# Optimization experiments

Measured on AMD Instinct MI355X. Metric: run time of the kernel, lower is better.

The kernel has to match this reference:

```python
import jax, jax.numpy as jnp
import numpy as np

NEG_INF = -1e30  # stands in for float('-inf') masked_fill; safe under softmax
MAX_ITERS = 6


def setup_inputs() -> dict:
    key = jax.random.key(0)
    ks = jax.random.split(key, 8)
    B, T, D, Dp, E = 8, 1500, 1536, 1024, 192
    s = lambda fan_in: 1.0 / np.sqrt(fan_in)
    return {
        "h": jax.random.normal(ks[0], (B, T, D), jnp.float32),
        "W1": jax.random.normal(ks[1], (3 * D, Dp), jnp.float32) * s(3 * D),
        "Wc": jax.random.normal(ks[2], (D, Dp), jnp.float32) * s(D),
        "W2": jax.random.normal(ks[3], (Dp, D), jnp.float32) * s(Dp),
        "b2": jnp.zeros((D,), jnp.float32),
        "w0": jax.random.normal(ks[4], (2 * D, E), jnp.float32) * s(2 * D),
        "b0": jnp.zeros((E,), jnp.float32),
        "Wstop": jax.random.normal(ks[5], (2 * D, 1), jnp.float32) * s(2 * D),
        "bstop": jnp.zeros((1,), jnp.float32),
        "threshold": jnp.full((1,), 0.5, jnp.float32),
        "C0": jnp.zeros((D,), jnp.float32),
    }


def _weighted_stats(h, a):
    # h: [B,T,D], a broadcastable to [B,T,D]
    mu = jnp.sum(a * h, axis=1)                         # [B,D]
    second = jnp.sum(a * h * h, axis=1)                 # [B,D]
    sigma = jnp.sqrt(jnp.clip(second - mu * mu, 1e-8))
    return mu, sigma


def reference(h, W1, Wc, W2, b2, w0, b0, Wstop, bstop, threshold, C0):
    B, T, D = h.shape
    th = threshold[0]

    # a_init = 1/T is constant across iterations -> hoist uniform stats and W1(e)
    mu0, sigma0 = _weighted_stats(h, jnp.float32(1.0 / T))          # [B,D]
    e = jnp.concatenate(
        [h,
         jnp.broadcast_to(mu0[:, None, :], (B, T, D)),
         jnp.broadcast_to(sigma0[:, None, :], (B, T, D))], axis=-1)  # [B,T,3D]
    base = jnp.einsum('btk,kp->btp', e, W1)                          # [B,T,Dp]

    energy_mask = jnp.mean(h * h, axis=-1) > 1e-4                    # [B,T]

    C = jnp.broadcast_to(C0[None, :], (B, D))
    stop = jnp.zeros((B,), bool)
    mask = jnp.ones((B, MAX_ITERS), bool)
    iters = jnp.arange(MAX_ITERS)

    embs, probs = [], []
    for i in range(MAX_ITERS):
        out1 = base + (C @ Wc)[:, None, :]                           # [B,T,Dp]
        out2 = jax.nn.relu(out1) @ W2 + b2                           # [B,T,D]
        att_raw = jnp.mean(out2, axis=-1)                            # [B,T]
        att_raw = jnp.where(energy_mask, att_raw, NEG_INF)
        A = jax.nn.softmax(att_raw, axis=-1)
        A = A / (jnp.sum(A, axis=1, keepdims=True) + 1e-8)

        # NOTE: faithful to source -- second weighted_stats uses out2 ('a'), not A
        mu_p, sigma_p = _weighted_stats(h, out2)                     # [B,D]
        emb = jnp.concatenate([mu_p, sigma_p], axis=-1) @ w0 + b0    # [B,E]
        emb = emb / jnp.maximum(
            jnp.linalg.norm(emb, axis=-1, keepdims=True), 1e-12)

        active = (~stop).astype(h.dtype)[:, None]
        C = C + active * (jnp.einsum('bt,btd->bd', A, h) / T)

        z = jnp.concatenate([jnp.sum(A[:, :, None] * out2, axis=1), C], axis=-1)
        p = jax.nn.sigmoid(z @ Wstop + bstop)[:, 0]                  # [B]

        newly = p < th
        mask = mask & ~(newly[:, None] & (iters[None, :] >= i))
        stop = stop | newly
        embs.append(emb)
        probs.append(p)

    E = jnp.stack(embs, axis=1)                                      # [B,6,E]
    E = E * mask[:, :, None].astype(E.dtype)
    P = jnp.stack(probs, axis=1)                                     # [B,6]
    return E, P
```

## Files before the change

### kernel.cpp

```cpp
#include <hip/hip_runtime.h>
#include <math.h>

#define NB 8
#define NT 1500
#define ND 1536
#define NP 1024
#define NE 192
#define NITER 6
#define NEGINF -1e30f

typedef __attribute__((ext_vector_type(8))) short bf16x8;
typedef __attribute__((ext_vector_type(4))) float f32x4;
typedef __attribute__((ext_vector_type(8))) unsigned short us16x8;

__device__ __forceinline__ unsigned short bf_rne(float x) {
    unsigned u = __float_as_uint(x);
    return (unsigned short)((u + 0x7FFFu + ((u >> 16) & 1u)) >> 16);
}
__device__ __forceinline__ float bf_f(unsigned short u) {
    return __uint_as_float(((unsigned)u) << 16);
}

__device__ __forceinline__ float block_reduce_sum(float v, float* red) {
    int tid = threadIdx.x;
    red[tid] = v; __syncthreads();
    for (int s = blockDim.x >> 1; s > 0; s >>= 1) {
        if (tid < s) red[tid] += red[tid + s];
        __syncthreads();
    }
    float r = red[0]; __syncthreads();
    return r;
}

__global__ void k_colstats(const float* __restrict__ h, float* __restrict__ sum1,
                           float* __restrict__ sum2) {
    int d = blockIdx.x * 256 + threadIdx.x;
    int b = blockIdx.y;
    int t0 = blockIdx.z * 125, t1 = t0 + 125;
    const float* hp = h + (size_t)b * NT * ND + d;
    float s = 0.f, s2 = 0.f;
    for (int t = t0; t < t1; ++t) { float v = hp[(size_t)t * ND]; s += v; s2 += v * v; }
    atomicAdd(&sum1[b * ND + d], s);
    atomicAdd(&sum2[b * ND + d], s2);
}

__global__ void k_stats_fin(float* __restrict__ mu0, float* __restrict__ sig0) {
    int i = blockIdx.x * 256 + threadIdx.x;
    float mu = mu0[i] * (1.f / NT);
    float sec = sig0[i] * (1.f / NT);
    mu0[i] = mu;
    sig0[i] = sqrtf(fmaxf(sec - mu * mu, 1e-8f));
}

__global__ void k_w2r(const float* __restrict__ W2, const float* __restrict__ b2,
                      float* __restrict__ w2r, float* __restrict__ b2m) {
    __shared__ float red[256];
    int p = blockIdx.x;
    float s = 0.f;
    if (p < NP) {
        const float* row = W2 + (size_t)p * ND;
        for (int d = threadIdx.x; d < ND; d += 256) s += row[d];
        s = block_reduce_sum(s, red);
        if (threadIdx.x == 0) w2r[p] = s * (1.f / ND);
    } else {
        for (int d = threadIdx.x; d < ND; d += 256) s += b2[d];
        s = block_reduce_sum(s, red);
        if (threadIdx.x == 0) b2m[0] = s * (1.f / ND);
    }
}

__global__ void k_biasb(const float* __restrict__ W1, const float* __restrict__ mu0,
                        const float* __restrict__ sig0, float* __restrict__ biasb) {
    int p = blockIdx.x * 256 + threadIdx.x;
    int d0 = blockIdx.y * 16, d1 = d0 + 16;
    float acc[NB];
#pragma unroll
    for (int b = 0; b < NB; ++b) acc[b] = 0.f;
    for (int d = d0; d < d1; ++d) {
        float wa = W1[(size_t)(ND + d) * NP + p];
        float wb = W1[(size_t)(2 * ND + d) * NP + p];
#pragma unroll
        for (int b = 0; b < NB; ++b)
            acc[b] += mu0[b * ND + d] * wa + sig0[b * ND + d] * wb;
    }
#pragma unroll
    for (int b = 0; b < NB; ++b) atomicAdd(&biasb[b * NP + p], acc[b]);
}

__global__ void k_init(float* __restrict__ C, const float* __restrict__ C0,
                       float* __restrict__ stopf) {
    int d = blockIdx.x * 256 + threadIdx.x;
    int b = blockIdx.y;
    C[b * ND + d] = C0[d];
    if (blockIdx.x == 0 && threadIdx.x == 0) stopf[b] = 0.f;
}

__global__ void k_split_w(const float* __restrict__ W, int ldw, int kcnt,
                          unsigned short* __restrict__ th, unsigned short* __restrict__ tl) {
    __shared__ float t[128][33];
    int nt = blockIdx.x, kc = blockIdx.y, tid = threadIdx.x;
    int col = tid & 127, kh = tid >> 7;
    const float* wp = W + (size_t)(kc * 32 + kh) * ldw + nt * 128 + col;
#pragma unroll
    for (int i = 0; i < 16; ++i)
        t[col][kh + 2 * i] = wp[(size_t)(2 * i) * ldw];
    __syncthreads();
    int r = tid >> 1;
    int swz = (r >> 1) & 3;
    size_t tb = ((size_t)nt * kcnt + kc) * 4096;
#pragma unroll
    for (int j = 0; j < 2; ++j) {
        int so = (tid & 1) * 2 + j;
        int s = so ^ swz;
        us16x8 hv, lv;
#pragma unroll
        for (int q = 0; q < 8; ++q) {
            float x = t[r][s * 8 + q];
            unsigned short hh = bf_rne(x);
            hv[q] = hh;
            lv[q] = bf_rne(x - bf_f(hh));
        }
        *(us16x8*)&th[tb + r * 32 + so * 8] = hv;
        *(us16x8*)&tl[tb + r * 32 + so * 8] = lv;
    }
}

__global__ void k_split_h(const float* __restrict__ h, unsigned short* __restrict__ th,
                          float* __restrict__ energy) {
    int tr = blockIdx.x, kc = blockIdx.y, b = blockIdx.z;
    int tid = threadIdx.x;
    int r = tid >> 1, quad = tid & 1;
    int row = tr * 128 + r;
    bool ok = row < NT;
    size_t tb = ((size_t)(b * 12 + tr) * 48 + kc) * 4096;
    const float* hp = h + ((size_t)b * NT + (ok ? row : 0)) * ND + kc * 32 + quad * 16;
    int swz = (r >> 1) & 3;
    float es = 0.f;
#pragma unroll
    for (int half = 0; half < 2; ++half) {
        us16x8 hv;
#pragma unroll
        for (int j = 0; j < 2; ++j) {
            float x0 = 0.f, x1 = 0.f, x2 = 0.f, x3 = 0.f;
            if (ok) {
                float4 v = *(const float4*)(hp + half * 8 + j * 4);
                x0 = v.x; x1 = v.y; x2 = v.z; x3 = v.w;
                es += x0 * x0 + x1 * x1 + x2 * x2 + x3 * x3;
            }
            hv[j * 4 + 0] = bf_rne(x0); hv[j * 4 + 1] = bf_rne(x1);
            hv[j * 4 + 2] = bf_rne(x2); hv[j * 4 + 3] = bf_rne(x3);
        }
        int off = r * 32 + (((quad * 2 + half) ^ swz) << 3);
        *(us16x8*)&th[tb + off] = hv;
    }
    es += __shfl_xor(es, 1);
    if (ok && quad == 0) atomicAdd(&energy[b * NT + row], es);
}

__global__ void k_relu_att(const unsigned short* __restrict__ base16,
                           const float* __restrict__ cvec, const float* __restrict__ w2r,
                           unsigned short* __restrict__ th, float* __restrict__ att) {
    int tr = blockIdx.x, kc = blockIdx.y, b = blockIdx.z;
    int tid = threadIdx.x;
    int r = tid >> 1, quad = tid & 1;
    int row = tr * 128 + r;
    bool ok = row < NT;
    size_t tb = ((size_t)(b * 12 + tr) * 32 + kc) * 4096;
    const unsigned short* bp = base16 + ((size_t)b * NT + (ok ? row : 0)) * NP + kc * 32 + quad * 16;
    const float* cv = cvec + b * NP + kc * 32 + quad * 16;
    const float* wr = w2r + kc * 32 + quad * 16;
    int swz = (r >> 1) & 3;
    float asum = 0.f;
#pragma unroll
    for (int half = 0; half < 2; ++half) {
        us16x8 bv = (us16x8){0, 0, 0, 0, 0, 0, 0, 0};
        if (ok) bv = *(const us16x8*)(bp + half * 8);
        us16x8 hv;
#pragma unroll
        for (int j = 0; j < 2; ++j) {
            float4 c4 = *(const float4*)(cv + half * 8 + j * 4);
            float4 w4 = *(const float4*)(wr + half * 8 + j * 4);
            float x0 = fmaxf(bf_f(bv[j * 4 + 0]) + c4.x, 0.f);
            float x1 = fmaxf(bf_f(bv[j * 4 + 1]) + c4.y, 0.f);
            float x2 = fmaxf(bf_f(bv[j * 4 + 2]) + c4.z, 0.f);
            float x3 = fmaxf(bf_f(bv[j * 4 + 3]) + c4.w, 0.f);
            if (ok) asum += x0 * w4.x + x1 * w4.y + x2 * w4.z + x3 * w4.w;
            hv[j * 4 + 0] = bf_rne(x0); hv[j * 4 + 1] = bf_rne(x1);
            hv[j * 4 + 2] = bf_rne(x2); hv[j * 4 + 3] = bf_rne(x3);
        }
        int off = r * 32 + (((quad * 2 + half) ^ swz) << 3);
        *(us16x8*)&th[tb + off] = hv;
    }
    asum += __shfl_xor(asum, 1);
    if (ok && quad == 0) atomicAdd(&att[b * NT + row], asum);
}

__global__ __launch_bounds__(256, 4) void k_gemm_relu(
    const unsigned short* __restrict__ ht, const unsigned short* __restrict__ at_h,
    const unsigned short* __restrict__ bt_h, const float* __restrict__ b2,
    const float* __restrict__ Aw, float* __restrict__ part) {
    constexpr int KC = NP / 32;
    __shared__ __align__(16) unsigned short As[2][4096];
    __shared__ __align__(16) unsigned short Bs[2][4096];
    int flat = blockIdx.x + 12 * (blockIdx.y + 12 * blockIdx.z);
    int swzf = (flat & 7) * 144 + (flat >> 3);
    int tr = swzf % 12, nt = (swzf / 12) % 12, b = swzf / 144;
    int tid = threadIdx.x;
    int lane = tid & 63, w = tid >> 6;
    int wr = w >> 1, wc = w & 1;
    int l15 = lane & 15, kg = lane >> 4;
    int sw = (l15 >> 1) & 3;
    f32x4 acc[4][4];
#pragma unroll
    for (int m = 0; m < 4; ++m)
#pragma unroll
        for (int n = 0; n < 4; ++n) acc[m][n] = (f32x4){0.f, 0.f, 0.f, 0.f};
    int aoff[4], boff[4];
#pragma unroll
    for (int m = 0; m < 4; ++m) aoff[m] = (wr * 64 + m * 16 + l15) * 32 + ((kg ^ sw) << 3);
#pragma unroll
    for (int n = 0; n < 4; ++n) boff[n] = (wc * 64 + n * 16 + l15) * 32 + ((kg ^ sw) << 3);

    const unsigned short* ga = at_h + ((size_t)(b * 12 + tr) * KC) * 4096 + lane * 8;
    const unsigned short* gb = bt_h + ((size_t)nt * KC) * 4096 + lane * 8;

    auto stage = [&](int buf, int kc) {
#pragma unroll
        for (int c = 0; c < 4; ++c) {
            int seg = w * 4 + c;
            int part_ = seg & 7;
            const unsigned short* src = ((seg >> 3) == 0 ? ga : gb) + (size_t)kc * 4096 + part_ * 512;
            unsigned short* dst = ((seg >> 3) == 0 ? &As[buf][0] : &Bs[buf][0]) + part_ * 512;
            __builtin_amdgcn_global_load_lds(src, dst, 16, 0, 0);
        }
    };

    stage(0, 0);
    __syncthreads();
    int cur = 0;
    for (int kc = 0; kc < KC; ++kc) {
        if (kc + 1 < KC) stage(cur ^ 1, kc + 1);
        bf16x8 af[4], bfr[4];
#pragma unroll
        for (int m = 0; m < 4; ++m) af[m] = *(const bf16x8*)&As[cur][aoff[m]];
#pragma unroll
        for (int n = 0; n < 4; ++n) bfr[n] = *(const bf16x8*)&Bs[cur][boff[n]];
#pragma unroll
        for (int n = 0; n < 4; ++n)
#pragma unroll
            for (int m = 0; m < 4; ++m)
                acc[m][n] = __builtin_amdgcn_mfma_f32_16x16x32_bf16(af[m], bfr[n], acc[m][n], 0, 0, 0);
        __syncthreads();
        cur ^= 1;
    }

    int rowb = tr * 128 + wr * 64 + (kg << 2);
    int colb = nt * 128 + wc * 64 + l15;
    const unsigned short* htb = ht + (size_t)(b * 12 + tr) * 48 * 4096;
    float b2c[4];
#pragma unroll
    for (int n = 0; n < 4; ++n) b2c[n] = b2[colb + n * 16];
    float pm[4] = {0, 0, 0, 0}, ps2[4] = {0, 0, 0, 0}, pza[4] = {0, 0, 0, 0}, pah[4] = {0, 0, 0, 0};
#pragma unroll
    for (int m = 0; m < 4; ++m) {
#pragma unroll
        for (int q = 0; q < 4; ++q) {
            int row = rowb + m * 16 + q;
            int r_in = wr * 64 + (kg << 2) + m * 16 + q;
            bool ok = row < NT;
            float okf = ok ? 1.f : 0.f;
            float a = Aw[b * NT + (ok ? row : (NT - 1))] * okf;
            int rsw = (r_in >> 1) & 3;
#pragma unroll
            for (int n = 0; n < 4; ++n) {
                int col = colb + n * 16;
                float hv = bf_f(htb[(size_t)(col >> 5) * 4096 + r_in * 32 +
                                    ((((col & 31) >> 3) ^ rsw) << 3) + (col & 7)]) * okf;
                float o2 = acc[m][n][q] + b2c[n];
                pm[n] = fmaf(o2, hv, pm[n]);
                ps2[n] = fmaf(o2 * hv, hv, ps2[n]);
                pza[n] = fmaf(a, o2, pza[n]);
                pah[n] = fmaf(a, hv, pah[n]);
            }
        }
    }
#pragma unroll
    for (int n = 0; n < 4; ++n) {
        pm[n] += __shfl_xor(pm[n], 16); pm[n] += __shfl_xor(pm[n], 32);
        ps2[n] += __shfl_xor(ps2[n], 16); ps2[n] += __shfl_xor(ps2[n], 32);
        pza[n] += __shfl_xor(pza[n], 16); pza[n] += __shfl_xor(pza[n], 32);
        pah[n] += __shfl_xor(pah[n], 16); pah[n] += __shfl_xor(pah[n], 32);
        if (kg == 0) {
            int col = colb + n * 16;
            size_t pb = (((size_t)(tr * 2 + wr) * NB + b) * 4) * ND;
            part[pb + 0 * (size_t)ND + col] = pm[n];
            part[pb + 1 * (size_t)ND + col] = ps2[n];
            part[pb + 2 * (size_t)ND + col] = pza[n];
            part[pb + 3 * (size_t)ND + col] = pah[n];
        }
    }
}

__global__ void k_redsum(const float* __restrict__ part, float* __restrict__ red4) {
    int idx = blockIdx.x * 256 + threadIdx.x;
    int b = idx / ND, d = idx % ND;
    float s0 = 0.f, s1 = 0.f, s2 = 0.f, s3 = 0.f;
    for (int s = 0; s < 24; ++s) {
        const float* p = part + (((size_t)s * NB + b) * 4) * ND + d;
        s0 += p[0];
        s1 += p[(size_t)ND];
        s2 += p[2 * (size_t)ND];
        s3 += p[3 * (size_t)ND];
    }
    red4[idx] = s0;
    red4[(size_t)NB * ND + idx] = s1;
    red4[3 * (size_t)NB * ND + idx] = s2;
    red4[2 * (size_t)NB * ND + idx] = s3;
}

__global__ __launch_bounds__(256, 3) void k_gemm_base(
    const unsigned short* __restrict__ ht, const unsigned short* __restrict__ bt_h,
    const unsigned short* __restrict__ bt_l, const float* __restrict__ biasb,
    unsigned short* __restrict__ Out16) {
    constexpr int KC2 = ND / 64;
    __shared__ __align__(16) unsigned short As[8192];
    __shared__ __align__(16) unsigned short Bh_s[8192];
    __shared__ __align__(16) unsigned short Bl_s[8192];
    int flat = blockIdx.x + 12 * (blockIdx.y + 8 * blockIdx.z);
    int swzf = (flat & 7) * 96 + (flat >> 3);
    int tr = swzf % 12, nt = (swzf / 12) % 8, b = swzf / 96;
    int tid = threadIdx.x;
    int lane = tid & 63, w = tid >> 6;
    int wr = w >> 1, wc = w & 1;
    int l15 = lane & 15, kg = lane >> 4;
    int sw = (l15 >> 1) & 3;
    f32x4 acc[4][4];
#pragma unroll
    for (int m = 0; m < 4; ++m)
#pragma unroll
        for (int n = 0; n < 4; ++n) acc[m][n] = (f32x4){0.f, 0.f, 0.f, 0.f};
    int aoff[4], boff[4];
#pragma unroll
    for (int m = 0; m < 4; ++m) aoff[m] = (wr * 64 + m * 16 + l15) * 32 + ((kg ^ sw) << 3);
#pragma unroll
    for (int n = 0; n < 4; ++n) boff[n] = (wc * 64 + n * 16 + l15) * 32 + ((kg ^ sw) << 3);

    const unsigned short* ga = ht + ((size_t)(b * 12 + tr) * 48) * 4096 + lane * 8;
    const unsigned short* gbh = bt_h + ((size_t)nt * 48) * 4096 + lane * 8;
    const unsigned short* gbl = bt_l + ((size_t)nt * 48) * 4096 + lane * 8;

    for (int kc2 = 0; kc2 < KC2; ++kc2) {
#pragma unroll
        for (int c = 0; c < 12; ++c) {
            int seg = w * 12 + c;
            int part = seg & 15, mat = seg >> 4;
            const unsigned short* src =
                (mat == 0 ? ga : mat == 1 ? gbh : gbl) + (size_t)kc2 * 8192 + part * 512;
            unsigned short* dst =
                (mat == 0 ? &As[0] : mat == 1 ? &Bh_s[0] : &Bl_s[0]) + part * 512;
            __builtin_amdgcn_global_load_lds(src, dst, 16, 0, 0);
        }
        __syncthreads();
#pragma unroll
        for (int half = 0; half < 2; ++half) {
            int ho = half * 4096;
            bf16x8 af[4];
#pragma unroll
            for (int m = 0; m < 4; ++m) af[m] = *(const bf16x8*)&As[ho + aoff[m]];
#pragma unroll
            for (int n = 0; n < 4; ++n) {
                bf16x8 bh = *(const bf16x8*)&Bh_s[ho + boff[n]];
                bf16x8 bl = *(const bf16x8*)&Bl_s[ho + boff[n]];
#pragma unroll
                for (int m = 0; m < 4; ++m) {
                    acc[m][n] = __builtin_amdgcn_mfma_f32_16x16x32_bf16(af[m], bh, acc[m][n], 0, 0, 0);
                    acc[m][n] = __builtin_amdgcn_mfma_f32_16x16x32_bf16(af[m], bl, acc[m][n], 0, 0, 0);
                }
            }
        }
        __syncthreads();
    }

    int rowb = tr * 128 + wr * 64 + (kg << 2);
    int colb = nt * 128 + wc * 64 + l15;
#pragma unroll
    for (int m = 0; m < 4; ++m)
#pragma unroll
        for (int q = 0; q < 4; ++q) {
            int row = rowb + m * 16 + q;
            if (row < NT) {
                unsigned short* orow = Out16 + ((size_t)b * NT + row) * NP;
#pragma unroll
                for (int n = 0; n < 4; ++n)
                    orow[colb + n * 16] =
                        bf_rne(acc[m][n][q] + biasb[b * NP + colb + n * 16]);
            }
        }
}

__global__ void k_cvec(const float* __restrict__ C, const float* __restrict__ Wc,
                       float* __restrict__ cvec) {
    int p = blockIdx.x * 256 + threadIdx.x;
    int d0 = blockIdx.y * 48, d1 = d0 + 48;
    float acc[NB];
#pragma unroll
    for (int b = 0; b < NB; ++b) acc[b] = 0.f;
    for (int d = d0; d < d1; ++d) {
        float wc = Wc[(size_t)d * NP + p];
#pragma unroll
        for (int b = 0; b < NB; ++b) acc[b] += C[b * ND + d] * wc;
    }
#pragma unroll
    for (int b = 0; b < NB; ++b) atomicAdd(&cvec[b * NP + p], acc[b]);
}

__global__ void k_softmax(const float* __restrict__ att, const float* __restrict__ energy,
                          const float* __restrict__ b2m, float* __restrict__ A) {
    __shared__ float red[256];
    int b = blockIdx.x, tid = threadIdx.x;
    float bm = b2m[0];
    const float* x = att + (size_t)b * NT;
    const float* en = energy + (size_t)b * NT;
    float* a = A + (size_t)b * NT;
    float mx = -3.4e38f;
    for (int t = tid; t < NT; t += 256) {
        float v = (en[t] * (1.f / ND) > 1e-4f) ? x[t] + bm : NEGINF;
        mx = fmaxf(mx, v);
    }
    red[tid] = mx; __syncthreads();
    for (int s = 128; s > 0; s >>= 1) {
        if (tid < s) red[tid] = fmaxf(red[tid], red[tid + s]);
        __syncthreads();
    }
    mx = red[0]; __syncthreads();
    float sm = 0.f;
    for (int t = tid; t < NT; t += 256) {
        float v = (en[t] * (1.f / ND) > 1e-4f) ? x[t] + bm : NEGINF;
        float e = expf(v - mx); a[t] = e; sm += e;
    }
    float s1 = block_reduce_sum(sm, red);
    float inv1 = 1.f / s1;
    float sm2 = 0.f;
    for (int t = tid; t < NT; t += 256) { float v = a[t] * inv1; a[t] = v; sm2 += v; }
    float s2 = block_reduce_sum(sm2, red);
    float inv2 = 1.f / (s2 + 1e-8f);
    for (int t = tid; t < NT; t += 256) a[t] *= inv2;
}

__global__ void k_embacc(const float* __restrict__ red4, const float* __restrict__ w0,
                         float* __restrict__ embt) {
    __shared__ float mus[NB][48], sgs[NB][48];
    int e = threadIdx.x;
    int d0 = blockIdx.x * 48;
    const float* mup = red4;
    const float* s2p = red4 + (size_t)NB * ND;
    for (int idx = e; idx < NB * 48; idx += 192) {
        int b = idx / 48, dd = idx % 48;
        float mu = mup[b * ND + d0 + dd];
        mus[b][dd] = mu;
        sgs[b][dd] = sqrtf(fmaxf(s2p[b * ND + d0 + dd] - mu * mu, 1e-8f));
    }
    __syncthreads();
    float acc[NB];
#pragma unroll
    for (int b = 0; b < NB; ++b) acc[b] = 0.f;
    for (int dd = 0; dd < 48; ++dd) {
        float wa = w0[(size_t)(d0 + dd) * NE + e];
        float wb = w0[(size_t)(ND + d0 + dd) * NE + e];
#pragma unroll
        for (int b = 0; b < NB; ++b)
            acc[b] += mus[b][dd] * wa + sgs[b][dd] * wb;
    }
#pragma unroll
    for (int b = 0; b < NB; ++b) atomicAdd(&embt[b * NE + e], acc[b]);
}

__global__ void k_tail2(const float* __restrict__ red4, const float* __restrict__ embt,
                        const float* __restrict__ b0, const float* __restrict__ Wstop,
                        const float* __restrict__ bstop, const float* __restrict__ thr,
                        float* __restrict__ Cb, float* __restrict__ stopf,
                        float* __restrict__ Eout, float* __restrict__ Pout, int iter) {
    __shared__ float red[256];
    __shared__ float liveflag;
    int b = blockIdx.x, tid = threadIdx.x;
    const float* Ahb = red4 + (size_t)2 * NB * ND + b * ND;
    const float* zAb = red4 + (size_t)3 * NB * ND + b * ND;
    float active = (stopf[b] > 0.5f) ? 0.f : 1.f;
    float dsum = 0.f;
    for (int d = tid; d < ND; d += 256) {
        float Cn = Cb[b * ND + d] + active * (Ahb[d] * (1.f / NT));
        Cb[b * ND + d] = Cn;
        dsum += zAb[d] * Wstop[d] + Cn * Wstop[ND + d];
    }
    float s = block_reduce_sum(dsum, red);
    if (tid == 0) {
        float logit = s + bstop[0];
        float p = 1.f / (1.f + expf(-logit));
        Pout[b * NITER + iter] = p;
        bool newly = p < thr[0];
        if (newly) stopf[b] = 1.f;
        liveflag = (active > 0.5f && !newly) ? 1.f : 0.f;
    }
    __syncthreads();
    float live = liveflag;
    float emb = (tid < NE) ? (embt[b * NE + tid] + b0[tid]) : 0.f;
    float nrm = block_reduce_sum(emb * emb, red);
    float sc = live / fmaxf(sqrtf(nrm), 1e-12f);
    if (tid < NE) Eout[((size_t)b * NITER + iter) * NE + tid] = emb * sc;
}

extern "C" void kernel_launch(void* const* d_in, const int* in_sizes, int n_in,
                              void* d_out, int out_size, void* d_ws, size_t ws_size,
                              hipStream_t stream) {
    const float* h = (const float*)d_in[0];
    const float* W1 = (const float*)d_in[1];
    const float* Wc = (const float*)d_in[2];
    const float* W2 = (const float*)d_in[3];
    const float* b2 = (const float*)d_in[4];
    const float* w0 = (const float*)d_in[5];
    const float* b0 = (const float*)d_in[6];
    const float* Wstop = (const float*)d_in[7];
    const float* bstop = (const float*)d_in[8];
    const float* thr = (const float*)d_in[9];
    const float* C0 = (const float*)d_in[10];

    float* Eout = (float*)d_out;
    float* Pout = Eout + (size_t)NB * NITER * NE;

    char* wsb = (char*)d_ws;
    size_t off = 0;
    auto alloc = [&](size_t bytes) -> void* {
        void* p = wsb + off; off += (bytes + 15) & ~(size_t)15; return p;
    };

    unsigned short* base16 = (unsigned short*)alloc((size_t)NB * NT * NP * 2);
    unsigned short* rel_h = (unsigned short*)alloc((size_t)NB * 12 * 32 * 4096 * 2);
    unsigned short* ht_h = (unsigned short*)alloc((size_t)NB * 12 * 48 * 4096 * 2);
    unsigned short* w1t_h = (unsigned short*)alloc((size_t)8 * 48 * 4096 * 2);
    unsigned short* w1t_l = (unsigned short*)alloc((size_t)8 * 48 * 4096 * 2);
    unsigned short* w2t_h = (unsigned short*)alloc((size_t)12 * 32 * 4096 * 2);
    unsigned short* w2t_l = (unsigned short*)alloc((size_t)12 * 32 * 4096 * 2);
    size_t pz = (size_t)2 * NB * ND + NB * NT + NB * NP;
    float* mu0 = (float*)alloc(pz * 4);
    float* sig0 = mu0 + NB * ND;
    float* energy = sig0 + NB * ND;
    float* biasb = energy + NB * NT;
    float* w2r = (float*)alloc(NP * 4);
    float* b2m = (float*)alloc(16);
    size_t zelems = (size_t)NB * NP + NB * NT + NB * NE;
    float* cvec = (float*)alloc(zelems * 4);
    float* att = cvec + NB * NP;
    float* embt = att + NB * NT;
    float* red4 = (float*)alloc((size_t)4 * NB * ND * 4);
    float* part = (float*)alloc((size_t)24 * NB * 4 * ND * 4);
    float* Abuf = (float*)alloc(NB * NT * 4);
    float* Cb = (float*)alloc(NB * ND * 4);
    float* stopf = (float*)alloc(32);
    size_t zero_bytes = zelems * 4;

    hipMemsetAsync(mu0, 0, pz * 4, stream);
    k_colstats<<<dim3(ND / 256, NB, 12), 256, 0, stream>>>(h, mu0, sig0);
    k_stats_fin<<<dim3(NB * ND / 256), 256, 0, stream>>>(mu0, sig0);
    k_w2r<<<dim3(NP + 1), 256, 0, stream>>>(W2, b2, w2r, b2m);
    k_biasb<<<dim3(4, 96), 256, 0, stream>>>(W1, mu0, sig0, biasb);
    k_split_w<<<dim3(8, 48), 256, 0, stream>>>(W1, NP, 48, w1t_h, w1t_l);
    k_split_w<<<dim3(12, 32), 256, 0, stream>>>(W2, ND, 32, w2t_h, w2t_l);
    k_split_h<<<dim3(12, 48, NB), 256, 0, stream>>>(h, ht_h, energy);
    k_gemm_base<<<dim3(12, 8, NB), 256, 0, stream>>>(ht_h, w1t_h, w1t_l, biasb, base16);
    k_init<<<dim3(ND / 256, NB), 256, 0, stream>>>(Cb, C0, stopf);

    for (int i = 0; i < NITER; ++i) {
        hipMemsetAsync(cvec, 0, zero_bytes, stream);
        k_cvec<<<dim3(4, 32), 256, 0, stream>>>(Cb, Wc, cvec);
        k_relu_att<<<dim3(12, 32, NB), 256, 0, stream>>>(base16, cvec, w2r, rel_h, att);
        k_softmax<<<dim3(NB), 256, 0, stream>>>(att, energy, b2m, Abuf);
        k_gemm_relu<<<dim3(12, 12, NB), 256, 0, stream>>>(
            ht_h, rel_h, w2t_h, b2, Abuf, part);
        k_redsum<<<dim3(48), 256, 0, stream>>>(part, red4);
        k_embacc<<<dim3(32), 192, 0, stream>>>(red4, w0, embt);
        k_tail2<<<dim3(NB), 256, 0, stream>>>(red4, embt, b0, Wstop, bstop, thr,
                                              Cb, stopf, Eout, Pout, i);
    }
}
```

Measured before the change: 1.107 ms.

## Fuse relu(base+cvec) into GEMM A-tile staging, drop relu tile buffer

```diff
diff --git a/kernel.cpp b/kernel.cpp
--- a/kernel.cpp
+++ b/kernel.cpp
@@ -157,51 +157,41 @@
     if (ok && quad == 0) atomicAdd(&energy[b * NT + row], es);
 }
 
-__global__ void k_relu_att(const unsigned short* __restrict__ base16,
-                           const float* __restrict__ cvec, const float* __restrict__ w2r,
-                           unsigned short* __restrict__ th, float* __restrict__ att) {
-    int tr = blockIdx.x, kc = blockIdx.y, b = blockIdx.z;
-    int tid = threadIdx.x;
-    int r = tid >> 1, quad = tid & 1;
-    int row = tr * 128 + r;
-    bool ok = row < NT;
-    size_t tb = ((size_t)(b * 12 + tr) * 32 + kc) * 4096;
-    const unsigned short* bp = base16 + ((size_t)b * NT + (ok ? row : 0)) * NP + kc * 32 + quad * 16;
-    const float* cv = cvec + b * NP + kc * 32 + quad * 16;
-    const float* wr = w2r + kc * 32 + quad * 16;
-    int swz = (r >> 1) & 3;
-    float asum = 0.f;
-#pragma unroll
-    for (int half = 0; half < 2; ++half) {
-        us16x8 bv = (us16x8){0, 0, 0, 0, 0, 0, 0, 0};
-        if (ok) bv = *(const us16x8*)(bp + half * 8);
-        us16x8 hv;
-#pragma unroll
-        for (int j = 0; j < 2; ++j) {
-            float4 c4 = *(const float4*)(cv + half * 8 + j * 4);
-            float4 w4 = *(const float4*)(wr + half * 8 + j * 4);
-            float x0 = fmaxf(bf_f(bv[j * 4 + 0]) + c4.x, 0.f);
-            float x1 = fmaxf(bf_f(bv[j * 4 + 1]) + c4.y, 0.f);
-            float x2 = fmaxf(bf_f(bv[j * 4 + 2]) + c4.z, 0.f);
-            float x3 = fmaxf(bf_f(bv[j * 4 + 3]) + c4.w, 0.f);
-            if (ok) asum += x0 * w4.x + x1 * w4.y + x2 * w4.z + x3 * w4.w;
-            hv[j * 4 + 0] = bf_rne(x0); hv[j * 4 + 1] = bf_rne(x1);
-            hv[j * 4 + 2] = bf_rne(x2); hv[j * 4 + 3] = bf_rne(x3);
-        }
-        int off = r * 32 + (((quad * 2 + half) ^ swz) << 3);
-        *(us16x8*)&th[tb + off] = hv;
-    }
-    asum += __shfl_xor(asum, 1);
-    if (ok && quad == 0) atomicAdd(&att[b * NT + row], asum);
+__global__ void k_att(const unsigned short* __restrict__ base16,
+                      const float* __restrict__ cvec, const float* __restrict__ w2r,
+                      float* __restrict__ att) {
+    __shared__ float cv_sh[NP], wr_sh[NP];
+    int blk = blockIdx.x, b = blockIdx.y;
+    int tid = threadIdx.x, lane = tid & 63, wv = tid >> 6;
+    for (int i = tid; i < NP / 4; i += 256) {
+        ((float4*)cv_sh)[i] = ((const float4*)(cvec + (size_t)b * NP))[i];
+        ((float4*)wr_sh)[i] = ((const float4*)w2r)[i];
+    }
+    __syncthreads();
+    int row = blk * 4 + wv;
+    const unsigned short* bp = base16 + ((size_t)b * NT + row) * NP + lane * 16;
+    us16x8 v0 = *(const us16x8*)bp;
+    us16x8 v1 = *(const us16x8*)(bp + 8);
+    float s = 0.f;
+#pragma unroll
+    for (int j = 0; j < 8; ++j)
+        s += fmaxf(bf_f(v0[j]) + cv_sh[lane * 16 + j], 0.f) * wr_sh[lane * 16 + j];
+#pragma unroll
+    for (int j = 0; j < 8; ++j)
+        s += fmaxf(bf_f(v1[j]) + cv_sh[lane * 16 + 8 + j], 0.f) * wr_sh[lane * 16 + 8 + j];
+#pragma unroll
+    for (int d = 1; d < 64; d <<= 1) s += __shfl_xor(s, d);
+    if (lane == 0) att[b * NT + row] = s;
 }
 
 __global__ __launch_bounds__(256, 4) void k_gemm_relu(
-    const unsigned short* __restrict__ ht, const unsigned short* __restrict__ at_h,
-    const unsigned short* __restrict__ bt_h, const float* __restrict__ b2,
-    const float* __restrict__ Aw, float* __restrict__ part) {
+    const unsigned short* __restrict__ base16, const float* __restrict__ cvec,
+    const unsigned short* __restrict__ ht, const unsigned short* __restrict__ bt_h,
+    const float* __restrict__ b2, const float* __restrict__ Aw, float* __restrict__ part) {
     constexpr int KC = NP / 32;
     __shared__ __align__(16) unsigned short As[2][4096];
     __shared__ __align__(16) unsigned short Bs[2][4096];
+    __shared__ float cv_sh[NP];
     int flat = blockIdx.x + 12 * (blockIdx.y + 12 * blockIdx.z);
     int swzf = (flat & 7) * 144 + (flat >> 3);
     int tr = swzf % 12, nt = (swzf / 12) % 12, b = swzf / 144;
@@ -221,25 +211,61 @@
 #pragma unroll
     for (int n = 0; n < 4; ++n) boff[n] = (wc * 64 + n * 16 + l15) * 32 + ((kg ^ sw) << 3);
 
-    const unsigned short* ga = at_h + ((size_t)(b * 12 + tr) * KC) * 4096 + lane * 8;
     const unsigned short* gb = bt_h + ((size_t)nt * KC) * 4096 + lane * 8;
 
-    auto stage = [&](int buf, int kc) {
-#pragma unroll
-        for (int c = 0; c < 4; ++c) {
-            int seg = w * 4 + c;
-            int part_ = seg & 7;
-            const unsigned short* src = ((seg >> 3) == 0 ? ga : gb) + (size_t)kc * 4096 + part_ * 512;
-            unsigned short* dst = ((seg >> 3) == 0 ? &As[buf][0] : &Bs[buf][0]) + part_ * 512;
+    int r2 = tid >> 1, quad = tid & 1;
+    int arow = tr * 128 + r2;
+    int rowc = arow < NT ? arow : (NT - 1);
+    int aswz = (r2 >> 1) & 3;
+    const unsigned short* ap = base16 + ((size_t)b * NT + rowc) * NP + quad * 16;
+
+    for (int i = tid; i < NP / 4; i += 256)
+        ((float4*)cv_sh)[i] = ((const float4*)(cvec + (size_t)b * NP))[i];
+    __syncthreads();
+
+    auto stageB = [&](int buf, int kc) {
+#pragma unroll
+        for (int c = 0; c < 2; ++c) {
+            int seg = w * 2 + c;
+            const unsigned short* src = gb + (size_t)kc * 4096 + seg * 512;
+            unsigned short* dst = &Bs[buf][0] + seg * 512;
             __builtin_amdgcn_global_load_lds(src, dst, 16, 0, 0);
         }
     };
-
-    stage(0, 0);
+    auto loadA = [&](int kc, us16x8* raw) {
+        raw[0] = *(const us16x8*)(ap + kc * 32);
+        raw[1] = *(const us16x8*)(ap + kc * 32 + 8);
+    };
+    auto writeA = [&](int buf, const us16x8* raw, int kc) {
+#pragma unroll
+        for (int half = 0; half < 2; ++half) {
+            us16x8 hv;
+#pragma unroll
+            for (int j = 0; j < 8; ++j) {
+                float x = bf_f(raw[half][j]) + cv_sh[kc * 32 + quad * 16 + half * 8 + j];
+                hv[j] = bf_rne(fmaxf(x, 0.f));
+            }
+            int so = quad * 2 + half;
+            int off = r2 * 32 + ((so ^ aswz) << 3);
+            *(us16x8*)&As[buf][off] = hv;
+        }
+    };
+
+    {
+        us16x8 raw0[2];
+        stageB(0, 0);
+        loadA(0, raw0);
+        writeA(0, raw0, 0);
+    }
     __syncthreads();
     int cur = 0;
     for (int kc = 0; kc < KC; ++kc) {
-        if (kc + 1 < KC) stage(cur ^ 1, kc + 1);
+        bool np = kc + 1 < KC;
+        us16x8 rawn[2];
+        if (np) {
+            stageB(cur ^ 1, kc + 1);
+            loadA(kc + 1, rawn);
+        }
         bf16x8 af[4], bfr[4];
 #pragma unroll
         for (int m = 0; m < 4; ++m) af[m] = *(const bf16x8*)&As[cur][aoff[m]];
@@ -250,6 +276,7 @@
 #pragma unroll
             for (int m = 0; m < 4; ++m)
                 acc[m][n] = __builtin_amdgcn_mfma_f32_16x16x32_bf16(af[m], bfr[n], acc[m][n], 0, 0, 0);
+        if (np) writeA(cur ^ 1, rawn, kc + 1);
         __syncthreads();
         cur ^= 1;
     }
@@ -534,7 +561,6 @@
     };
 
     unsigned short* base16 = (unsigned short*)alloc((size_t)NB * NT * NP * 2);
-    unsigned short* rel_h = (unsigned short*)alloc((size_t)NB * 12 * 32 * 4096 * 2);
     unsigned short* ht_h = (unsigned short*)alloc((size_t)NB * 12 * 48 * 4096 * 2);
     unsigned short* w1t_h = (unsigned short*)alloc((size_t)8 * 48 * 4096 * 2);
     unsigned short* w1t_l = (unsigned short*)alloc((size_t)8 * 48 * 4096 * 2);
@@ -547,10 +573,10 @@
     float* biasb = energy + NB * NT;
     float* w2r = (float*)alloc(NP * 4);
     float* b2m = (float*)alloc(16);
-    size_t zelems = (size_t)NB * NP + NB * NT + NB * NE;
+    size_t zelems = (size_t)NB * NP + NB * NE;
     float* cvec = (float*)alloc(zelems * 4);
-    float* att = cvec + NB * NP;
-    float* embt = att + NB * NT;
+    float* embt = cvec + NB * NP;
+    float* att = (float*)alloc((size_t)NB * NT * 4);
     float* red4 = (float*)alloc((size_t)4 * NB * ND * 4);
     float* part = (float*)alloc((size_t)24 * NB * 4 * ND * 4);
     float* Abuf = (float*)alloc(NB * NT * 4);
@@ -572,10 +598,10 @@
     for (int i = 0; i < NITER; ++i) {
         hipMemsetAsync(cvec, 0, zero_bytes, stream);
         k_cvec<<<dim3(4, 32), 256, 0, stream>>>(Cb, Wc, cvec);
-        k_relu_att<<<dim3(12, 32, NB), 256, 0, stream>>>(base16, cvec, w2r, rel_h, att);
+        k_att<<<dim3(375, NB), 256, 0, stream>>>(base16, cvec, w2r, att);
         k_softmax<<<dim3(NB), 256, 0, stream>>>(att, energy, b2m, Abuf);
         k_gemm_relu<<<dim3(12, 12, NB), 256, 0, stream>>>(
-            ht_h, rel_h, w2t_h, b2, Abuf, part);
+            base16, cvec, ht_h, w2t_h, b2, Abuf, part);
         k_redsum<<<dim3(48), 256, 0, stream>>>(part, red4);
         k_embacc<<<dim3(32), 192, 0, stream>>>(red4, w0, embt);
         k_tail2<<<dim3(NB), 256, 0, stream>>>(red4, embt, b0, Wstop, bstop, thr,
```

New measurement: 1.197 ms. +8.1%, slower.
